# Kernel optimization log

Measured on AMD Instinct MI355X. Metric: run time of the kernel, lower is better.

Reference implementation:

```python
import jax, jax.numpy as jnp
import numpy as np

B, T, D = 4, 2048, 1024
H, HD = 16, 64  # num_heads, head_size; H*HD == D
DFF = 4 * D
EPS = 1e-5

def _ln(x, g, b):
    mu = jnp.mean(x, axis=-1, keepdims=True)
    var = jnp.mean(jnp.square(x - mu), axis=-1, keepdims=True)
    return (x - mu) * jax.lax.rsqrt(var + EPS) * g + b

def setup_inputs() -> dict:
    key = jax.random.key(0)
    ks = jax.random.split(key, 12)
    s = lambda fan_in: 1.0 / np.sqrt(fan_in)
    return {
        "x": jax.random.normal(ks[0], (B, T, D), jnp.float32),
        "Wq": jax.random.normal(ks[1], (H, D, HD), jnp.float32) * s(D),
        "Wk": jax.random.normal(ks[2], (H, D, HD), jnp.float32) * s(D),
        "Wv": jax.random.normal(ks[3], (H, D, HD), jnp.float32) * s(D),
        "Wo": jax.random.normal(ks[4], (D, D), jnp.float32) * s(D),
        "bo": jax.random.normal(ks[5], (D,), jnp.float32) * 0.01,
        "W1": jax.random.normal(ks[6], (D, DFF), jnp.float32) * s(D),
        "b1": jax.random.normal(ks[7], (DFF,), jnp.float32) * 0.01,
        "W2": jax.random.normal(ks[8], (DFF, D), jnp.float32) * s(DFF),
        "b2": jax.random.normal(ks[9], (D,), jnp.float32) * 0.01,
        "g1": jnp.ones((D,), jnp.float32),
        "be1": jnp.zeros((D,), jnp.float32),
        "g2": jnp.ones((D,), jnp.float32),
        "be2": jnp.zeros((D,), jnp.float32),
    }

def reference(x, Wq, Wk, Wv, Wo, bo, W1, b1, W2, b2, g1, be1, g2, be2):
    # pre-LN attention
    h = _ln(x, g1, be1)                                   # [B,T,D]
    q = jnp.einsum('btd,hde->bhte', h, Wq)                # [B,H,T,HD]
    k = jnp.einsum('btd,hde->bhte', h, Wk)
    v = jnp.einsum('btd,hde->bhte', h, Wv)
    scores = jnp.einsum('bhte,bhse->bhts', q, k) * (HD ** -0.5)  # [B,H,T,T]
    mask = jnp.tril(jnp.ones((T, T), bool))
    scores = jnp.where(mask, scores, -jnp.inf)
    attn = jax.nn.softmax(scores, axis=-1)
    ctx = jnp.einsum('bhts,bhse->bhte', attn, v)          # [B,H,T,HD]
    ctx = ctx.transpose(0, 2, 1, 3).reshape(B, T, D)      # concat heads
    x = x + jnp.einsum('btd,de->bte', ctx, Wo) + bo
    # pre-LN FFN
    h2 = _ln(x, g2, be2)
    ff = jax.nn.relu(jnp.einsum('btd,df->btf', h2, W1) + b1)
    x = x + jnp.einsum('btf,fd->btd', ff, W2) + b2
    return x
```

## Files before the change

kernel.cpp:

```cpp
#include <hip/hip_runtime.h>
#include <stdint.h>

#define B_ 4
#define T_ 2048
#define D_ 1024
#define H_ 16
#define HD_ 64
#define DFF_ 4096
#define M_ (B_ * T_)

typedef __bf16 bf16x8 __attribute__((ext_vector_type(8)));
typedef float f32x4 __attribute__((ext_vector_type(4)));

__device__ __forceinline__ uint16_t f2bf(float f) {
  union { float f; uint32_t u; } v;
  v.f = f;
  uint32_t r = v.u + 0x7FFF + ((v.u >> 16) & 1);
  return (uint16_t)(r >> 16);
}

#define GLD_LDS(gp, lp)                                                        \
  __builtin_amdgcn_global_load_lds(                                            \
      (const __attribute__((address_space(1))) void*)(gp),                     \
      (__attribute__((address_space(3))) void*)(lp), 16, 0, 0)

__global__ __launch_bounds__(256) void ln_bf16(const float* __restrict__ x,
                                               const float* __restrict__ gamma,
                                               const float* __restrict__ beta,
                                               uint16_t* __restrict__ out) {
  __shared__ float red[4];
  const int tid = threadIdx.x;
  const size_t row = blockIdx.x;
  const float4 v = ((const float4*)(x + row * D_))[tid];
  float s = v.x + v.y + v.z + v.w;
#pragma unroll
  for (int off = 32; off >= 1; off >>= 1) s += __shfl_xor(s, off, 64);
  if ((tid & 63) == 0) red[tid >> 6] = s;
  __syncthreads();
  const float mean = (red[0] + red[1] + red[2] + red[3]) * (1.0f / D_);
  const float d0 = v.x - mean, d1 = v.y - mean, d2 = v.z - mean, d3 = v.w - mean;
  float ss = d0 * d0 + d1 * d1 + d2 * d2 + d3 * d3;
#pragma unroll
  for (int off = 32; off >= 1; off >>= 1) ss += __shfl_xor(ss, off, 64);
  __syncthreads();
  if ((tid & 63) == 0) red[tid >> 6] = ss;
  __syncthreads();
  const float var = (red[0] + red[1] + red[2] + red[3]) * (1.0f / D_);
  const float rstd = rsqrtf(var + 1e-5f);
  const float4 g = ((const float4*)gamma)[tid];
  const float4 b = ((const float4*)beta)[tid];
  ushort4 o;
  o.x = f2bf(d0 * rstd * g.x + b.x);
  o.y = f2bf(d1 * rstd * g.y + b.y);
  o.z = f2bf(d2 * rstd * g.z + b.z);
  o.w = f2bf(d3 * rstd * g.w + b.w);
  ((ushort4*)(out + row * D_))[tid] = o;
}

__global__ __launch_bounds__(256) void transpose_cast(const float* __restrict__ in,
                                                      uint16_t* __restrict__ out,
                                                      int R, int C) {
  __shared__ float tile[32][33];
  const int tx = threadIdx.x & 31, ty = threadIdx.x >> 5;
  const int c0 = blockIdx.x * 32, r0 = blockIdx.y * 32;
#pragma unroll
  for (int i = 0; i < 32; i += 8)
    tile[ty + i][tx] = in[(size_t)(r0 + ty + i) * C + c0 + tx];
  __syncthreads();
#pragma unroll
  for (int i = 0; i < 32; i += 8)
    out[(size_t)(c0 + ty + i) * R + r0 + tx] = f2bf(tile[tx][ty + i]);
}

__global__ __launch_bounds__(256) void qkv_wt(const float* __restrict__ Wq,
                                              const float* __restrict__ Wk,
                                              const float* __restrict__ Wv,
                                              uint16_t* __restrict__ out) {
  __shared__ float tile[32][33];
  const int tx = threadIdx.x & 31, ty = threadIdx.x >> 5;
  const int z = blockIdx.z, which = z >> 4, hh = z & 15;
  const float* W = (which == 0) ? Wq : ((which == 1) ? Wk : Wv);
  const float* in = W + (size_t)hh * D_ * HD_;
  const int e0 = blockIdx.x * 32, d0 = blockIdx.y * 32;
#pragma unroll
  for (int i = 0; i < 32; i += 8)
    tile[ty + i][tx] = in[(size_t)(d0 + ty + i) * HD_ + e0 + tx];
  __syncthreads();
#pragma unroll
  for (int i = 0; i < 32; i += 8)
    out[((size_t)(which * 1024 + hh * 64) + e0 + ty + i) * D_ + d0 + tx] =
        f2bf(tile[tx][ty + i]);
}

__global__ __launch_bounds__(256) void gemm_bf16(const uint16_t* __restrict__ A,
                                                 const uint16_t* __restrict__ Bt,
                                                 void* __restrict__ C,
                                                 const float* __restrict__ bias,
                                                 const float* __restrict__ resid,
                                                 int M, int N, int K, int lda,
                                                 int ldb, int flags) {
  __shared__ __align__(16) uint16_t As[128 * 32];
  __shared__ __align__(16) uint16_t Bs[128 * 32];
  const int tid = threadIdx.x;
  const int lane = tid & 63, w = tid >> 6;
  const int quad = lane >> 4, lr = lane & 15;
  const int wr = w >> 1, wc = w & 1;

  const int gn = N >> 8;
  const int pid = blockIdx.x;
  const int xcd = pid & 7, rid = pid >> 3;
  const int sm = rid & 3;
  const int t = rid >> 2;
  const int nt_loc = t % gn;
  const int ms = t / gn;
  const int mt = (xcd >> 1) * 16 + ms * 4 + sm;
  const int nt = (xcd & 1) * gn + nt_loc;
  const int bn0 = nt * 128, bm0 = mt * 128;

  f32x4 acc[4][4];
#pragma unroll
  for (int i = 0; i < 4; i++)
#pragma unroll
    for (int j = 0; j < 4; j++) acc[i][j] = f32x4{0.f, 0.f, 0.f, 0.f};

  const int s_sub = lane >> 2, s_slot = lane & 3;

  for (int k0 = 0; k0 < K; k0 += 32) {
#pragma unroll
    for (int i = 0; i < 2; i++) {
      const int r = w * 32 + i * 16 + s_sub;
      const int cg = s_slot ^ ((r >> 1) & 3);
      GLD_LDS(A + (size_t)(bm0 + r) * lda + k0 + cg * 8, As + (w * 32 + i * 16) * 32);
      GLD_LDS(Bt + (size_t)(bn0 + r) * ldb + k0 + cg * 8, Bs + (w * 32 + i * 16) * 32);
    }
    __syncthreads();

    bf16x8 af[4], bfr[4];
#pragma unroll
    for (int i = 0; i < 4; i++) {
      const int m = wr * 64 + i * 16 + lr;
      const int slot = quad ^ ((m >> 1) & 3);
      af[i] = *(const bf16x8*)(As + m * 32 + slot * 8);
    }
#pragma unroll
    for (int j = 0; j < 4; j++) {
      const int n = wc * 64 + j * 16 + lr;
      const int slot = quad ^ ((n >> 1) & 3);
      bfr[j] = *(const bf16x8*)(Bs + n * 32 + slot * 8);
    }
#pragma unroll
    for (int i = 0; i < 4; i++)
#pragma unroll
      for (int j = 0; j < 4; j++)
        acc[i][j] = __builtin_amdgcn_mfma_f32_16x16x32_bf16(af[i], bfr[j], acc[i][j], 0, 0, 0);
    __syncthreads();
  }

  const int base_m = bm0 + wr * 64 + quad * 4;
  const int base_n = bn0 + wc * 64 + lr;
#pragma unroll
  for (int i = 0; i < 4; i++) {
#pragma unroll
    for (int j = 0; j < 4; j++) {
      const int col = base_n + j * 16;
      const float bv = bias ? bias[col] : 0.f;
#pragma unroll
      for (int r = 0; r < 4; r++) {
        const size_t row = base_m + i * 16 + r;
        float v = acc[i][j][r] + bv;
        if (resid) v += resid[row * N + col];
        if (flags & 1) v = fmaxf(v, 0.f);
        if (flags & 2)
          ((uint16_t*)C)[row * N + col] = f2bf(v);
        else
          ((float*)C)[row * N + col] = v;
      }
    }
  }
}

__global__ __launch_bounds__(256) void v_transpose(const uint16_t* __restrict__ qkv,
                                                   uint16_t* __restrict__ vtb) {
  __shared__ __align__(16) uint16_t tile[64 * 72];
  const int tid = threadIdx.x;
  const int t0 = blockIdx.x * 64;
  const int bh = blockIdx.y;
  const int b = bh >> 4, h = bh & 15;
  const uint16_t* src = qkv + (size_t)b * T_ * 3072 + 2048 + h * 64;
#pragma unroll
  for (int u = 0; u < 2; u++) {
    const int uu = tid + u * 256;
    const int r = uu >> 3, c = uu & 7;
    *(int4*)(tile + r * 72 + c * 8) =
        *(const int4*)(src + (size_t)(t0 + r) * 3072 + c * 8);
  }
  __syncthreads();
  uint16_t* dst = vtb + ((size_t)bh * 64) * T_ + t0;
#pragma unroll
  for (int u = 0; u < 2; u++) {
    const int uu = tid + u * 256;
    const int e = uu >> 3, c2 = uu & 7;
    union { uint16_t u16[8]; int4 v; } tmp;
#pragma unroll
    for (int jj = 0; jj < 8; jj++) tmp.u16[jj] = tile[(c2 * 8 + jj) * 72 + e];
    *(int4*)(dst + (size_t)e * T_ + c2 * 8) = tmp.v;
  }
}

__global__ __launch_bounds__(256) void attn_mfma(const uint16_t* __restrict__ qkv,
                                                 const uint16_t* __restrict__ vtb,
                                                 uint16_t* __restrict__ ctx) {
  __shared__ __align__(16) uint16_t Ks[64 * 72];
  __shared__ __align__(16) uint16_t Vt[64 * 72];
  __shared__ __align__(16) uint16_t Ps[128 * 72];
  const int tid = threadIdx.x;
  const int lane = tid & 63, w = tid >> 6;
  const int quad = lane >> 4, lr = lane & 15;
  const int h = blockIdx.y, b = blockIdx.z;
  const uint16_t* base = qkv + (size_t)b * T_ * 3072 + h * 64;
  const uint16_t* vbase = vtb + ((size_t)(b * H_ + h) * 64) * T_;
  const int sr = tid >> 3, sc = tid & 7;

#pragma unroll
  for (int half = 0; half < 2; half++) {
    const int tq = (half == 0) ? (int)blockIdx.x : 15 - (int)blockIdx.x;
    const int q0 = tq * 128;

    bf16x8 aq[2][2];
#pragma unroll
    for (int i = 0; i < 2; i++)
#pragma unroll
      for (int ks = 0; ks < 2; ks++)
        aq[i][ks] = *(const bf16x8*)(base + (size_t)(q0 + w * 32 + i * 16 + lr) * 3072 +
                                     ks * 32 + quad * 8);

    f32x4 oacc[2][4];
#pragma unroll
    for (int i = 0; i < 2; i++)
#pragma unroll
      for (int j = 0; j < 4; j++) oacc[i][j] = f32x4{0.f, 0.f, 0.f, 0.f};
    float l_part[2] = {0.f, 0.f};

    const int row_min_w = q0 + w * 32;
    const int row_max_w = row_min_w + 31;
    const int nt = 2 * tq + 2;

    for (int st = 0; st < nt; st++) {
      __syncthreads();
#pragma unroll
      for (int u = 0; u < 2; u++) {
        const int r = sr + u * 32;
        *(int4*)(Ks + r * 72 + sc * 8) =
            *(const int4*)(base + 1024 + (size_t)(st * 64 + r) * 3072 + sc * 8);
        *(int4*)(Vt + r * 72 + sc * 8) =
            *(const int4*)(vbase + (size_t)r * T_ + st * 64 + sc * 8);
      }
      __syncthreads();

      if (st * 64 > row_max_w) continue;

      f32x4 sa[2][4];
#pragma unroll
      for (int i = 0; i < 2; i++)
#pragma unroll
        for (int sf = 0; sf < 4; sf++) sa[i][sf] = f32x4{0.f, 0.f, 0.f, 0.f};
#pragma unroll
      for (int ks = 0; ks < 2; ks++) {
        bf16x8 ak[4];
#pragma unroll
        for (int sf = 0; sf < 4; sf++)
          ak[sf] = *(const bf16x8*)(Ks + (sf * 16 + lr) * 72 + ks * 32 + quad * 8);
#pragma unroll
        for (int i = 0; i < 2; i++)
#pragma unroll
          for (int sf = 0; sf < 4; sf++)
            sa[i][sf] = __builtin_amdgcn_mfma_f32_16x16x32_bf16(ak[sf], aq[i][ks],
                                                                sa[i][sf], 0, 0, 0);
      }

#pragma unroll
      for (int i = 0; i < 2; i++) {
        const int mrow = q0 + w * 32 + i * 16 + lr;
#pragma unroll
        for (int sf = 0; sf < 4; sf++) {
          const int s0 = st * 64 + sf * 16 + quad * 4;
          float p[4];
#pragma unroll
          for (int r = 0; r < 4; r++) {
            float sv = sa[i][sf][r];
            if (s0 + r > mrow) sv = -1e30f;
            p[r] = exp2f(fmaf(sv, 0.18033688f, -28.8539008f));
            l_part[i] += p[r];
          }
          ushort4 pk;
          pk.x = f2bf(p[0]);
          pk.y = f2bf(p[1]);
          pk.z = f2bf(p[2]);
          pk.w = f2bf(p[3]);
          *(ushort4*)(Ps + (size_t)(w * 32 + i * 16 + lr) * 72 + sf * 16 + quad * 4) = pk;
        }
      }

#pragma unroll
      for (int ks = 0; ks < 2; ks++) {
        bf16x8 ap[2], bv[4];
#pragma unroll
        for (int i = 0; i < 2; i++)
          ap[i] = *(const bf16x8*)(Ps + (size_t)(w * 32 + i * 16 + lr) * 72 + ks * 32 +
                                   quad * 8);
#pragma unroll
        for (int j = 0; j < 4; j++)
          bv[j] = *(const bf16x8*)(Vt + (j * 16 + lr) * 72 + ks * 32 + quad * 8);
#pragma unroll
        for (int i = 0; i < 2; i++)
#pragma unroll
          for (int j = 0; j < 4; j++)
            oacc[i][j] =
                __builtin_amdgcn_mfma_f32_16x16x32_bf16(ap[i], bv[j], oacc[i][j], 0, 0, 0);
      }
    }

    float linv[2];
#pragma unroll
    for (int i = 0; i < 2; i++) {
      float l = l_part[i];
      l += __shfl_xor(l, 16, 64);
      l += __shfl_xor(l, 32, 64);
      linv[i] = 1.f / l;
    }
    uint16_t* ob =
        ctx + ((size_t)b * T_ + q0 + w * 32 + quad * 4) * D_ + h * 64 + lr;
#pragma unroll
    for (int i = 0; i < 2; i++)
#pragma unroll
      for (int r = 0; r < 4; r++) {
        const float inv = __shfl(linv[i], quad * 4 + r, 64);
#pragma unroll
        for (int j = 0; j < 4; j++)
          ob[(size_t)(i * 16 + r) * D_ + j * 16] = f2bf(oacc[i][j][r] * inv);
      }
  }
}

extern "C" void kernel_launch(void* const* d_in, const int* in_sizes, int n_in,
                              void* d_out, int out_size, void* d_ws, size_t ws_size,
                              hipStream_t stream) {
  const float* x = (const float*)d_in[0];
  const float* Wq = (const float*)d_in[1];
  const float* Wk = (const float*)d_in[2];
  const float* Wv = (const float*)d_in[3];
  const float* Wo = (const float*)d_in[4];
  const float* bo = (const float*)d_in[5];
  const float* W1 = (const float*)d_in[6];
  const float* b1 = (const float*)d_in[7];
  const float* W2 = (const float*)d_in[8];
  const float* b2 = (const float*)d_in[9];
  const float* g1 = (const float*)d_in[10];
  const float* be1 = (const float*)d_in[11];
  const float* g2 = (const float*)d_in[12];
  const float* be2 = (const float*)d_in[13];
  float* out = (float*)d_out;

  const size_t MB = 1024ull * 1024ull;
  if (ws_size < 200 * MB) return;
  char* ws = (char*)d_ws;
  uint16_t* hbuf = (uint16_t*)(ws + 0 * MB);
  uint16_t* wqkvt = (uint16_t*)(ws + 16 * MB);
  uint16_t* wot = (uint16_t*)(ws + 22 * MB);
  uint16_t* w1t = (uint16_t*)(ws + 24 * MB);
  uint16_t* w2t = (uint16_t*)(ws + 32 * MB);
  float* x1 = (float*)(ws + 40 * MB);
  uint16_t* qkvb = (uint16_t*)(ws + 72 * MB);
  uint16_t* ctxb = (uint16_t*)(ws + 120 * MB);
  uint16_t* vtb = (uint16_t*)(ws + 136 * MB);
  uint16_t* ffb = (uint16_t*)(ws + 136 * MB);

  qkv_wt<<<dim3(2, 32, 48), 256, 0, stream>>>(Wq, Wk, Wv, wqkvt);
  transpose_cast<<<dim3(32, 32), 256, 0, stream>>>(Wo, wot, 1024, 1024);
  transpose_cast<<<dim3(128, 32), 256, 0, stream>>>(W1, w1t, 1024, 4096);
  transpose_cast<<<dim3(32, 128), 256, 0, stream>>>(W2, w2t, 4096, 1024);

  ln_bf16<<<M_, 256, 0, stream>>>(x, g1, be1, hbuf);
  gemm_bf16<<<64 * 24, 256, 0, stream>>>(hbuf, wqkvt, qkvb, nullptr, nullptr, M_,
                                         3 * D_, D_, D_, D_, 2);
  v_transpose<<<dim3(T_ / 64, B_ * H_), 256, 0, stream>>>(qkvb, vtb);
  attn_mfma<<<dim3(8, H_, B_), 256, 0, stream>>>(qkvb, vtb, ctxb);
  gemm_bf16<<<64 * 8, 256, 0, stream>>>(ctxb, wot, x1, bo, x, M_, D_, D_, D_, D_, 0);
  ln_bf16<<<M_, 256, 0, stream>>>(x1, g2, be2, hbuf);
  gemm_bf16<<<64 * 32, 256, 0, stream>>>(hbuf, w1t, ffb, b1, nullptr, M_, DFF_, D_,
                                         D_, D_, 1 | 2);
  gemm_bf16<<<64 * 8, 256, 0, stream>>>(ffb, w2t, out, b2, x1, M_, D_, DFF_, DFF_,
                                        DFF_, 0);
}
```

Before: 600.1 us.

## Double GEMM K-tile to 64 with 8-slot XOR swizzle and grouped tile order

The bf16 GEMM kernel now stages a K-step of 64 per iteration instead of 32, with a new 8-way XOR swizzle for the LDS layout, and runs two MFMA sub-steps per barrier pair. This halves the number of __syncthreads and load rounds per output tile. The block-to-tile mapping also changes from an XCD-aware mapping to a simple grouping of 16 M-tiles per N column, which alters L2 locality across XCDs. LDS use per block doubles, which may reduce occupancy.

```diff
diff --git a/kernel.cpp b/kernel.cpp
--- a/kernel.cpp
+++ b/kernel.cpp
@@ -99,22 +99,20 @@
                                                  const float* __restrict__ resid,
                                                  int M, int N, int K, int lda,
                                                  int ldb, int flags) {
-  __shared__ __align__(16) uint16_t As[128 * 32];
-  __shared__ __align__(16) uint16_t Bs[128 * 32];
+  __shared__ __align__(16) uint16_t As[128 * 64];
+  __shared__ __align__(16) uint16_t Bs[128 * 64];
   const int tid = threadIdx.x;
   const int lane = tid & 63, w = tid >> 6;
   const int quad = lane >> 4, lr = lane & 15;
   const int wr = w >> 1, wc = w & 1;
 
-  const int gn = N >> 8;
+  const int n_tiles = N >> 7;
   const int pid = blockIdx.x;
-  const int xcd = pid & 7, rid = pid >> 3;
-  const int sm = rid & 3;
-  const int t = rid >> 2;
-  const int nt_loc = t % gn;
-  const int ms = t / gn;
-  const int mt = (xcd >> 1) * 16 + ms * 4 + sm;
-  const int nt = (xcd & 1) * gn + nt_loc;
+  const int grp = 16 * n_tiles;
+  const int gid = pid / grp;
+  const int rem = pid - gid * grp;
+  const int nt = rem / 16;
+  const int mt = gid * 16 + (rem - nt * 16);
   const int bn0 = nt * 128, bm0 = mt * 128;
 
   f32x4 acc[4][4];
@@ -123,36 +121,40 @@
 #pragma unroll
     for (int j = 0; j < 4; j++) acc[i][j] = f32x4{0.f, 0.f, 0.f, 0.f};
 
-  const int s_sub = lane >> 2, s_slot = lane & 3;
-
-  for (int k0 = 0; k0 < K; k0 += 32) {
-#pragma unroll
-    for (int i = 0; i < 2; i++) {
-      const int r = w * 32 + i * 16 + s_sub;
-      const int cg = s_slot ^ ((r >> 1) & 3);
-      GLD_LDS(A + (size_t)(bm0 + r) * lda + k0 + cg * 8, As + (w * 32 + i * 16) * 32);
-      GLD_LDS(Bt + (size_t)(bn0 + r) * ldb + k0 + cg * 8, Bs + (w * 32 + i * 16) * 32);
+  const int s_row = lane >> 3, s_slot = lane & 7;
+
+  for (int k0 = 0; k0 < K; k0 += 64) {
+#pragma unroll
+    for (int u = 0; u < 4; u++) {
+      const int r = w * 32 + u * 8 + s_row;
+      const int cg = s_slot ^ (r & 7);
+      GLD_LDS(A + (size_t)(bm0 + r) * lda + k0 + cg * 8, As + (w * 32 + u * 8) * 64);
+      GLD_LDS(Bt + (size_t)(bn0 + r) * ldb + k0 + cg * 8, Bs + (w * 32 + u * 8) * 64);
     }
     __syncthreads();
 
-    bf16x8 af[4], bfr[4];
-#pragma unroll
-    for (int i = 0; i < 4; i++) {
-      const int m = wr * 64 + i * 16 + lr;
-      const int slot = quad ^ ((m >> 1) & 3);
-      af[i] = *(const bf16x8*)(As + m * 32 + slot * 8);
-    }
-#pragma unroll
-    for (int j = 0; j < 4; j++) {
-      const int n = wc * 64 + j * 16 + lr;
-      const int slot = quad ^ ((n >> 1) & 3);
-      bfr[j] = *(const bf16x8*)(Bs + n * 32 + slot * 8);
-    }
-#pragma unroll
-    for (int i = 0; i < 4; i++)
-#pragma unroll
-      for (int j = 0; j < 4; j++)
-        acc[i][j] = __builtin_amdgcn_mfma_f32_16x16x32_bf16(af[i], bfr[j], acc[i][j], 0, 0, 0);
+#pragma unroll
+    for (int ks = 0; ks < 2; ks++) {
+      bf16x8 af[4], bfr[4];
+#pragma unroll
+      for (int i = 0; i < 4; i++) {
+        const int m = wr * 64 + i * 16 + lr;
+        const int slot = (ks * 4 + quad) ^ (m & 7);
+        af[i] = *(const bf16x8*)(As + m * 64 + slot * 8);
+      }
+#pragma unroll
+      for (int j = 0; j < 4; j++) {
+        const int n = wc * 64 + j * 16 + lr;
+        const int slot = (ks * 4 + quad) ^ (n & 7);
+        bfr[j] = *(const bf16x8*)(Bs + n * 64 + slot * 8);
+      }
+#pragma unroll
+      for (int i = 0; i < 4; i++)
+#pragma unroll
+        for (int j = 0; j < 4; j++)
+          acc[i][j] =
+              __builtin_amdgcn_mfma_f32_16x16x32_bf16(af[i], bfr[j], acc[i][j], 0, 0, 0);
+    }
     __syncthreads();
   }
 
```

Result: faster. 568.1 us (-5.3%).
